# Performance work log

Hardware: AMD Instinct MI355X
Metric: run time of the kernel (lower is better)

## Reference

```python
import jax, jax.numpy as jnp
import numpy as np

B, C, H, W = 512, 256, 9, 9
HEADS, K = 4, 9
D_K = C // HEADS
EPS = 1e-5


def setup_inputs() -> dict:
    key = jax.random.key(0)
    ks = jax.random.split(key, 8)
    s = 1.0 / np.sqrt(C)
    return {
        "x": jax.random.normal(ks[0], (B, C, H, W), jnp.float32),
        "wq": jax.random.normal(ks[1], (C, C), jnp.float32) * s,
        "bq": jax.random.normal(ks[2], (C,), jnp.float32) * s,
        "wk": jax.random.normal(ks[3], (C, C), jnp.float32) * s,
        "bk": jax.random.normal(ks[4], (C,), jnp.float32) * s,
        "wv": jax.random.normal(ks[5], (C, C), jnp.float32) * s,
        "bv": jax.random.normal(ks[6], (C,), jnp.float32) * s,
        "a": jax.random.normal(ks[7], (HEADS, D_K), jnp.float32),
        "gamma": jnp.ones((C,), jnp.float32),
        "beta": jnp.zeros((C,), jnp.float32),
    }


def reference(x, wq, bq, wk, bk, wv, bv, a, gamma, beta):
    N = H * W  # 81 tokens
    tokens = x.reshape(B, C, N).transpose(0, 2, 1)  # [B, N, C]

    # pairwise euclidean distances (cdist)
    sq = jnp.sum(tokens * tokens, axis=-1)  # [B, N]
    d2 = sq[:, :, None] + sq[:, None, :] - 2.0 * jnp.einsum("bnc,bmc->bnm", tokens, tokens)
    dist = jnp.sqrt(jnp.maximum(d2, 0.0))  # [B, N, N]

    # k nearest neighbors (smallest distance)
    _, idx = jax.lax.top_k(-dist, K)  # idx: [B, N, K]

    # gather neighbor features: [B, N, K, C]
    nbr = jax.vmap(lambda t, i: t[i])(tokens, idx)

    q = tokens @ wq.T + bq                      # [B, N, C]
    kf = nbr @ wk.T + bk                        # [B, N, K, C]
    comb = jax.nn.leaky_relu(q[:, :, None, :] + kf, 0.2)
    comb = comb.reshape(B, N, K, HEADS, D_K)
    scores = jnp.einsum("bnkhd,hd->bnkh", comb, a)
    attn = jax.nn.softmax(scores, axis=2)       # over K neighbors
    v = (nbr @ wv.T + bv).reshape(B, N, K, HEADS, D_K)
    out = jnp.einsum("bnkh,bnkhd->bnhd", attn, v).reshape(B, N, C)
    out = out.transpose(0, 2, 1).reshape(B, C, H, W)

    # BatchNorm2d (training-mode batch statistics, biased variance)
    mean = jnp.mean(out, axis=(0, 2, 3))
    var = jnp.var(out, axis=(0, 2, 3))
    bn = (out - mean[None, :, None, None]) * jax.lax.rsqrt(var + EPS)[None, :, None, None]
    bn = bn * gamma[None, :, None, None] + beta[None, :, None, None]
    return jax.nn.relu(bn + x)
```

## Files before the change

### kernel.cpp

```cpp
#include <hip/hip_runtime.h>
#include <hip/hip_bf16.h>

#define B_   512
#define C_   256
#define N_   81
#define M_   (B_ * N_)
#define KNN  9

typedef __attribute__((ext_vector_type(8))) short short8;
typedef __attribute__((ext_vector_type(4))) float f32x4;
typedef __attribute__((ext_vector_type(4))) ushort u16x4;

#define GLD16(g, l) __builtin_amdgcn_global_load_lds(                      \
    (const __attribute__((address_space(1))) void*)(g),                    \
    (__attribute__((address_space(3))) void*)(l), 16, 0, 0)

__device__ __forceinline__ float bf2f(ushort u) {
  union { uint i; float f; } c; c.i = (uint)u << 16; return c.f;
}
__device__ __forceinline__ ushort f2bf(float f) {
  __hip_bfloat16 h = __float2bfloat16(f); return *(ushort*)&h;
}

__global__ __launch_bounds__(256) void split_kernel(
    const float* __restrict__ x, ushort* __restrict__ tokb,
    char* __restrict__ hlbuf,
    const float* __restrict__ wq, const float* __restrict__ bq,
    const float* __restrict__ wk, const float* __restrict__ bk,
    const float* __restrict__ wv, const float* __restrict__ bv,
    ushort* __restrict__ wcat, float* __restrict__ bcat) {
  __shared__ __align__(16) float raw[32 * 81];
  const int bid = blockIdx.x;
  const int tid = threadIdx.x;
  if (bid >= 4096) {
    const int j = bid - 4096, c = tid;
    const int sel = j >> 8, jr = j & 255;
    const float* W  = sel == 0 ? wq : (sel == 1 ? wk : wv);
    const float* Bb = sel == 0 ? bq : (sel == 1 ? bk : bv);
    wcat[(size_t)j * 256 + c] = f2bf(W[jr * 256 + c]);
    if (c == 0) bcat[j] = Bb[jr];
    return;
  }
  const int b = bid >> 3, ch = bid & 7;
  const float* src = x + (size_t)b * (C_ * N_) + ch * 32 * N_;
#pragma unroll
  for (int it = 0; it < 3; ++it) {
    int e4 = tid + it * 256;
    if (e4 < 648) *(f32x4*)&raw[e4 * 4] = *(const f32x4*)&src[e4 * 4];
  }
  char* dst = hlbuf + (size_t)bid * 12288;
  for (int p = tid; p < 480; p += 256)
    *(uint*)(dst + (81 + p / 32) * 128 + (p & 31) * 4) = 0u;
  __syncthreads();
#pragma unroll
  for (int it = 0; it < 6; ++it) {
    int p = tid + it * 256;
    if (p < 1296) {
      int n = p >> 4, q = p & 15;
      float v0 = raw[(2 * q) * N_ + n];
      float v1 = raw[(2 * q + 1) * N_ + n];
      __hip_bfloat16 h0 = __float2bfloat16(v0);
      __hip_bfloat16 h1 = __float2bfloat16(v1);
      float r0 = v0 - __bfloat162float(h0);
      float r1 = v1 - __bfloat162float(h1);
      __hip_bfloat16 g0 = __float2bfloat16(r0);
      __hip_bfloat16 g1 = __float2bfloat16(r1);
      uint hp = (uint)(*(ushort*)&h0) | ((uint)(*(ushort*)&h1) << 16);
      uint lp = (uint)(*(ushort*)&g0) | ((uint)(*(ushort*)&g1) << 16);
      int off = (((q >> 2) << 4) ^ (((n >> 1) & 3) << 4)) + ((q & 3) << 2);
      int hs = (n & 1) << 6;
      *(uint*)(dst + n * 128 + hs + off) = hp;
      *(uint*)(dst + n * 128 + (hs ^ 64) + off) = lp;
      *(uint*)&tokb[((size_t)(b * N_ + n)) * 256 + ch * 32 + 2 * q] = hp;
    }
  }
}

__global__ __launch_bounds__(256) void knn_kernel(
    const char* __restrict__ hlbuf, int* __restrict__ knn_idx) {
  __shared__ __align__(16) char smem[31488];
  __shared__ float sqv[96];
  const int b = blockIdx.x;
  const int tid = threadIdx.x;
  const int w = tid >> 6, lane = tid & 63;
  const int wr = w >> 1, wc = w & 1;
  const int l15 = lane & 15;
  const int g16 = lane >> 4;

  const char* srcb = hlbuf + (size_t)b * 8 * 12288;

#pragma unroll
  for (int it = 0; it < 3; ++it) {
    int idx = it * 256 + tid;
    GLD16(srcb + idx * 16, smem + idx * 16);
  }

  f32x4 acc[3][3];
#pragma unroll
  for (int i = 0; i < 3; ++i)
#pragma unroll
    for (int j = 0; j < 3; ++j) acc[i][j] = {0.f, 0.f, 0.f, 0.f};

#pragma unroll
  for (int ch = 0; ch < 8; ++ch) {
    char* cur = smem + (ch & 1) * 12288;
    char* nxt = smem + ((ch + 1) & 1) * 12288;
    if (ch < 7) {
      const char* s2 = srcb + (size_t)(ch + 1) * 12288;
#pragma unroll
      for (int it = 0; it < 3; ++it) {
        int idx = it * 256 + tid;
        GLD16(s2 + idx * 16, nxt + idx * 16);
      }
      asm volatile("s_waitcnt vmcnt(3)" ::: "memory");
    } else {
      asm volatile("s_waitcnt vmcnt(0)" ::: "memory");
    }
    __builtin_amdgcn_s_barrier();
    __builtin_amdgcn_sched_barrier(0);
    short8 ah[3], al[3], bh[3], bl[3];
#pragma unroll
    for (int i = 0; i < 3; ++i) {
      int ra = wr * 48 + i * 16 + l15;
      int basea = ra * 128 + ((g16 << 4) ^ (((ra >> 1) & 3) << 4));
      int hsa = (ra & 1) << 6;
      ah[i] = *(const short8*)(cur + basea + hsa);
      al[i] = *(const short8*)(cur + basea + (hsa ^ 64));
      int rb = wc * 48 + i * 16 + l15;
      int baseb = rb * 128 + ((g16 << 4) ^ (((rb >> 1) & 3) << 4));
      int hsb = (rb & 1) << 6;
      bh[i] = *(const short8*)(cur + baseb + hsb);
      bl[i] = *(const short8*)(cur + baseb + (hsb ^ 64));
    }
#pragma unroll
    for (int i = 0; i < 3; ++i)
#pragma unroll
      for (int j = 0; j < 3; ++j) {
        acc[i][j] = __builtin_amdgcn_mfma_f32_16x16x32_bf16(
            ah[i], bh[j], acc[i][j], 0, 0, 0);
        acc[i][j] = __builtin_amdgcn_mfma_f32_16x16x32_bf16(
            ah[i], bl[j], acc[i][j], 0, 0, 0);
        acc[i][j] = __builtin_amdgcn_mfma_f32_16x16x32_bf16(
            al[i], bh[j], acc[i][j], 0, 0, 0);
        acc[i][j] = __builtin_amdgcn_mfma_f32_16x16x32_bf16(
            al[i], bl[j], acc[i][j], 0, 0, 0);
      }
    __builtin_amdgcn_sched_barrier(0);
    __builtin_amdgcn_s_barrier();
  }
  float* G = (float*)smem;
#pragma unroll
  for (int i = 0; i < 3; ++i) {
    const int row0 = wr * 48 + i * 16 + ((lane >> 4) << 2);
#pragma unroll
    for (int j = 0; j < 3; ++j) {
      const int col = wc * 48 + j * 16 + l15;
#pragma unroll
      for (int reg = 0; reg < 4; ++reg) {
        const int row = row0 + reg;
        if (row < N_) G[row * 97 + col] = acc[i][j][reg];
      }
    }
  }
  __syncthreads();
  if (tid < N_) sqv[tid] = G[tid * 97 + tid];
  __syncthreads();
  if (tid < N_) {
    const int n = tid;
    const float sn = sqv[n];
    const float* grow = &G[n * 97];
    float bd[KNN]; int bi[KNN];
#pragma unroll
    for (int k = 0; k < KNN; ++k) { bd[k] = 3.4e38f; bi[k] = 0; }
    for (int m = 0; m < N_; ++m) {
      float d2 = sn + sqv[m] - 2.f * grow[m];
      float wv = bd[0]; int wi = 0;
#pragma unroll
      for (int k = 1; k < KNN; ++k) {
        bool g_ = bd[k] > wv;
        wv = g_ ? bd[k] : wv;
        wi = g_ ? k : wi;
      }
      bool repl = d2 < wv;
#pragma unroll
      for (int k = 0; k < KNN; ++k) {
        bool here = repl & (wi == k);
        bd[k] = here ? d2 : bd[k];
        bi[k] = here ? m : bi[k];
      }
    }
#pragma unroll
    for (int k = 0; k < KNN; ++k)
      knn_idx[((size_t)b * N_ + n) * KNN + k] = bi[k];
  }
}

__global__ __launch_bounds__(256) void qkv_mfma_kernel(
    const ushort* __restrict__ tokb, const ushort* __restrict__ wcat,
    const float* __restrict__ bcat, ushort* __restrict__ qkvb) {
  __shared__ ushort At[128 * 64];
  __shared__ ushort Bt[128 * 64];
  const int bid = blockIdx.x;
  const int xcd = bid & 7, li = bid >> 3;
  const int mt = xcd * 41 + li / 6;
  if (mt >= 324) return;
  const int m0 = mt * 128;
  const int j0 = (li % 6) * 128;
  const int tid = threadIdx.x;
  const int w = tid >> 6, lane = tid & 63;
  const int wr = w >> 1, wc = w & 1;

  const char* pA[4]; const char* pB[4]; int oL[4];
#pragma unroll
  for (int it = 0; it < 4; ++it) {
    int o = (it * 256 + tid) * 16;
    int r = o >> 7, cp = o & 127;
    int cl = cp ^ ((r & 7) << 4);
    oL[it] = o;
    pA[it] = (const char*)tokb + ((size_t)(m0 + r) * 256) * 2 + cl;
    pB[it] = (const char*)wcat + ((size_t)(j0 + r) * 256) * 2 + cl;
  }

  f32x4 acc[4][4];
#pragma unroll
  for (int i = 0; i < 4; ++i)
#pragma unroll
    for (int j = 0; j < 4; ++j) acc[i][j] = {0.f, 0.f, 0.f, 0.f};

  const int l15 = lane & 15;
  const int sw = (lane & 7) << 4;
  const int kgrp = (lane >> 4) << 4;

  for (int k0 = 0; k0 < 256; k0 += 64) {
    __syncthreads();
#pragma unroll
    for (int it = 0; it < 4; ++it) {
      GLD16(pA[it] + k0 * 2, (char*)At + oL[it]);
      GLD16(pB[it] + k0 * 2, (char*)Bt + oL[it]);
    }
    __syncthreads();
#pragma unroll
    for (int kk = 0; kk < 2; ++kk) {
      const int cb = (kk * 64 + kgrp) ^ sw;
      short8 am[4], bn[4];
#pragma unroll
      for (int i = 0; i < 4; ++i) {
        const int ra = wr * 64 + i * 16 + l15;
        am[i] = *(const short8*)((const char*)At + ra * 128 + cb);
        const int rb = wc * 64 + i * 16 + l15;
        bn[i] = *(const short8*)((const char*)Bt + rb * 128 + cb);
      }
#pragma unroll
      for (int i = 0; i < 4; ++i)
#pragma unroll
        for (int j = 0; j < 4; ++j)
          acc[i][j] = __builtin_amdgcn_mfma_f32_16x16x32_bf16(
              am[i], bn[j], acc[i][j], 0, 0, 0);
    }
  }

#pragma unroll
  for (int j = 0; j < 4; ++j) {
    const int colj = j0 + wc * 64 + j * 16 + l15;
    const float bs = bcat[colj];
#pragma unroll
    for (int i = 0; i < 4; ++i) {
      const int rowm = m0 + wr * 64 + i * 16 + ((lane >> 4) << 2);
#pragma unroll
      for (int reg = 0; reg < 4; ++reg)
        qkvb[(size_t)(rowm + reg) * 768 + colj] = f2bf(acc[i][j][reg] + bs);
    }
  }
}

__global__ __launch_bounds__(256) void attn_kernel(
    const ushort* __restrict__ qkvc, const int* __restrict__ knn_idx,
    const float* __restrict__ a, ushort* __restrict__ qkvb) {
  const int nwg = M_ / 4;
  const int bid = blockIdx.x;
  const int swz = (bid & 7) * (nwg / 8) + (bid >> 3);
  const int w = threadIdx.x >> 6, lane = threadIdx.x & 63;
  const int m = swz * 4 + w;
  const int b = m / N_;
  const int bbase = b * N_;

  const u16x4 qu = *(const u16x4*)&qkvc[(size_t)m * 768 + lane * 4];
  const f32x4 a4 = *(const f32x4*)&a[lane * 4];
  float q4[4];
#pragma unroll
  for (int u = 0; u < 4; ++u) q4[u] = bf2f(qu[u]);

  float sc[KNN];
  int nb[KNN];
#pragma unroll
  for (int k = 0; k < KNN; ++k) {
    int nbk = knn_idx[(size_t)m * KNN + k];
    nbk = __builtin_amdgcn_readfirstlane(nbk);
    nb[k] = nbk;
    const ushort* krow = qkvc + (size_t)(bbase + nbk) * 768 + 256;
    const u16x4 ku = *(const u16x4*)&krow[lane * 4];
    float p = 0.f;
#pragma unroll
    for (int u = 0; u < 4; ++u) {
      float t = q4[u] + bf2f(ku[u]);
      t = fmaxf(t, 0.2f * t);
      p = __builtin_fmaf(t, a4[u], p);
    }
    p += __shfl_xor(p, 1, 16);
    p += __shfl_xor(p, 2, 16);
    p += __shfl_xor(p, 4, 16);
    p += __shfl_xor(p, 8, 16);
    sc[k] = p;
  }
  float mx = sc[0];
#pragma unroll
  for (int k = 1; k < KNN; ++k) mx = fmaxf(mx, sc[k]);
  float s = 0.f;
#pragma unroll
  for (int k = 0; k < KNN; ++k) {
    sc[k] = __builtin_amdgcn_exp2f((sc[k] - mx) * 1.44269504f);
    s += sc[k];
  }
  const float inv = __builtin_amdgcn_rcpf(s);
  f32x4 acc = {0.f, 0.f, 0.f, 0.f};
#pragma unroll
  for (int k = 0; k < KNN; ++k) {
    const ushort* vrow = qkvc + (size_t)(bbase + nb[k]) * 768 + 512;
    const u16x4 vu = *(const u16x4*)&vrow[lane * 4];
    const float wk_ = sc[k] * inv;
#pragma unroll
    for (int u = 0; u < 4; ++u)
      acc[u] = __builtin_fmaf(wk_, bf2f(vu[u]), acc[u]);
  }
  u16x4 o;
#pragma unroll
  for (int u = 0; u < 4; ++u) o[u] = f2bf(acc[u]);
  *(u16x4*)&qkvb[(size_t)m * 768 + lane * 4] = o;
}

__global__ __launch_bounds__(256) void bn_partial_kernel(
    const ushort* __restrict__ qkvb, float* __restrict__ ps,
    float* __restrict__ ps2) {
  const int g = blockIdx.x, c = threadIdx.x;
  float s = 0.f, s2 = 0.f;
  for (int r = 0; r < M_ / 256; ++r) {
    float v = bf2f(qkvb[((size_t)g * (M_ / 256) + r) * 768 + c]);
    s += v; s2 += v * v;
  }
  ps[g * 256 + c] = s;
  ps2[g * 256 + c] = s2;
}

__global__ __launch_bounds__(256) void bn_finalize_kernel(
    const float* __restrict__ ps, const float* __restrict__ ps2,
    const float* __restrict__ gamma, const float* __restrict__ beta,
    float* __restrict__ scale, float* __restrict__ shift) {
  const int c = threadIdx.x;
  float s = 0.f, s2 = 0.f;
  for (int g = 0; g < 256; ++g) { s += ps[g * 256 + c]; s2 += ps2[g * 256 + c]; }
  const float mean = s * (1.f / (float)M_);
  const float var = s2 * (1.f / (float)M_) - mean * mean;
  const float rstd = rsqrtf(var + 1e-5f);
  scale[c] = gamma[c] * rstd;
  shift[c] = beta[c] - mean * gamma[c] * rstd;
}

__global__ __launch_bounds__(256) void bn_apply_kernel(
    const ushort* __restrict__ qkvb, const float* __restrict__ x,
    const float* __restrict__ scale, const float* __restrict__ shift,
    float* __restrict__ y) {
  __shared__ float t[N_ * 65];
  const int b = blockIdx.x, tid = threadIdx.x;
  for (int c0 = 0; c0 < 256; c0 += 64) {
    __syncthreads();
    for (int e = tid; e < N_ * 64; e += 256) {
      int n = e >> 6, c = e & 63;
      t[n * 65 + c] = bf2f(qkvb[((size_t)b * N_ + n) * 768 + c0 + c]);
    }
    __syncthreads();
    for (int f = tid; f < 64 * N_; f += 256) {
      int c = f / N_, n = f - c * N_;
      float o = t[n * 65 + c];
      size_t gi = (size_t)b * (C_ * N_) + (size_t)(c0 + c) * N_ + n;
      float bn = o * scale[c0 + c] + shift[c0 + c];
      float v = bn + x[gi];
      y[gi] = v > 0.f ? v : 0.f;
    }
  }
}

extern "C" void kernel_launch(void* const* d_in, const int* in_sizes, int n_in,
                              void* d_out, int out_size, void* d_ws,
                              size_t ws_size, hipStream_t stream) {
  const float* x     = (const float*)d_in[0];
  const float* wq    = (const float*)d_in[1];
  const float* bq    = (const float*)d_in[2];
  const float* wk    = (const float*)d_in[3];
  const float* bk    = (const float*)d_in[4];
  const float* wv    = (const float*)d_in[5];
  const float* bv    = (const float*)d_in[6];
  const float* a     = (const float*)d_in[7];
  const float* gamma = (const float*)d_in[8];
  const float* beta  = (const float*)d_in[9];
  float* out = (float*)d_out;

  ushort* qkvb = (ushort*)d_ws;
  char*   hlbuf = (char*)qkvb;
  ushort* tokb = qkvb + (size_t)M_ * 768;
  ushort* wcat = tokb + (size_t)M_ * 256;
  float*  bcat = (float*)(wcat + 768 * 256);
  int*    kidx = (int*)(bcat + 768);
  float*  ps   = (float*)(kidx + (size_t)M_ * KNN);
  float*  ps2  = ps + 256 * 256;
  float*  scale = ps2 + 256 * 256;
  float*  shift = scale + 256;

  split_kernel<<<4096 + 768, 256, 0, stream>>>(
      x, tokb, hlbuf, wq, bq, wk, bk, wv, bv, wcat, bcat);
  knn_kernel<<<B_, 256, 0, stream>>>(hlbuf, kidx);
  qkv_mfma_kernel<<<1968, 256, 0, stream>>>(tokb, wcat, bcat, qkvb);
  attn_kernel<<<M_ / 4, 256, 0, stream>>>(qkvb, kidx, a, qkvb);
  bn_partial_kernel<<<256, 256, 0, stream>>>(qkvb, ps, ps2);
  bn_finalize_kernel<<<1, 256, 0, stream>>>(ps, ps2, gamma, beta, scale, shift);
  bn_apply_kernel<<<B_, 256, 0, stream>>>(qkvb, x, scale, shift, out);
}
```

Measured before the change: 166.0 us.

## Store only bf16 residual in split buffer; knn reads high part from tokb

The split kernel no longer writes an interleaved hi/lo staging buffer. It writes only the low (residual) bf16 halves in a compact 64-byte-per-row layout. The knn kernel now pulls the high halves straight from the existing tokb token buffer with a swizzled global-to-LDS load and places the lo halves in a separate LDS region, which cuts global write traffic and zero padding. The attention kernel also loads the 9 neighbour indices once across lanes and broadcasts each with readlane instead of issuing 9 scalar loads. One risk is that the padding rows (81..95) of the lo buffer are no longer zeroed, so the knn tile may read stale data there, and the hi part for those rows now comes from the next batch's tokens.

```diff
diff --git a/kernel.cpp b/kernel.cpp
--- a/kernel.cpp
+++ b/kernel.cpp
@@ -24,7 +24,7 @@
 
 __global__ __launch_bounds__(256) void split_kernel(
     const float* __restrict__ x, ushort* __restrict__ tokb,
-    char* __restrict__ hlbuf,
+    char* __restrict__ lobuf,
     const float* __restrict__ wq, const float* __restrict__ bq,
     const float* __restrict__ wk, const float* __restrict__ bk,
     const float* __restrict__ wv, const float* __restrict__ bv,
@@ -48,9 +48,7 @@
     int e4 = tid + it * 256;
     if (e4 < 648) *(f32x4*)&raw[e4 * 4] = *(const f32x4*)&src[e4 * 4];
   }
-  char* dst = hlbuf + (size_t)bid * 12288;
-  for (int p = tid; p < 480; p += 256)
-    *(uint*)(dst + (81 + p / 32) * 128 + (p & 31) * 4) = 0u;
+  char* dst = lobuf + (size_t)bid * 6144;
   __syncthreads();
 #pragma unroll
   for (int it = 0; it < 6; ++it) {
@@ -68,16 +66,15 @@
       uint hp = (uint)(*(ushort*)&h0) | ((uint)(*(ushort*)&h1) << 16);
       uint lp = (uint)(*(ushort*)&g0) | ((uint)(*(ushort*)&g1) << 16);
       int off = (((q >> 2) << 4) ^ (((n >> 1) & 3) << 4)) + ((q & 3) << 2);
-      int hs = (n & 1) << 6;
-      *(uint*)(dst + n * 128 + hs + off) = hp;
-      *(uint*)(dst + n * 128 + (hs ^ 64) + off) = lp;
+      *(uint*)(dst + n * 64 + off) = lp;
       *(uint*)&tokb[((size_t)(b * N_ + n)) * 256 + ch * 32 + 2 * q] = hp;
     }
   }
 }
 
 __global__ __launch_bounds__(256) void knn_kernel(
-    const char* __restrict__ hlbuf, int* __restrict__ knn_idx) {
+    const ushort* __restrict__ tokb, const char* __restrict__ lobuf,
+    int* __restrict__ knn_idx) {
   __shared__ __align__(16) char smem[31488];
   __shared__ float sqv[96];
   const int b = blockIdx.x;
@@ -87,12 +84,19 @@
   const int l15 = lane & 15;
   const int g16 = lane >> 4;
 
-  const char* srcb = hlbuf + (size_t)b * 8 * 12288;
+  const char* tb = (const char*)(tokb + (size_t)b * N_ * 256);
+  const char* lb = lobuf + (size_t)b * 8 * 6144;
 
 #pragma unroll
   for (int it = 0; it < 3; ++it) {
     int idx = it * 256 + tid;
-    GLD16(srcb + idx * 16, smem + idx * 16);
+    if (idx < 384) {
+      int n = idx >> 2, gp = idx & 3;
+      int g = gp ^ ((n >> 1) & 3);
+      GLD16(tb + (size_t)n * 512 + (g << 4), smem + idx * 16);
+    } else {
+      GLD16(lb + (idx - 384) * 16, smem + idx * 16);
+    }
   }
 
   f32x4 acc[3][3];
@@ -106,11 +110,18 @@
     char* cur = smem + (ch & 1) * 12288;
     char* nxt = smem + ((ch + 1) & 1) * 12288;
     if (ch < 7) {
-      const char* s2 = srcb + (size_t)(ch + 1) * 12288;
 #pragma unroll
       for (int it = 0; it < 3; ++it) {
         int idx = it * 256 + tid;
-        GLD16(s2 + idx * 16, nxt + idx * 16);
+        if (idx < 384) {
+          int n = idx >> 2, gp = idx & 3;
+          int g = gp ^ ((n >> 1) & 3);
+          GLD16(tb + (size_t)n * 512 + (ch + 1) * 64 + (g << 4),
+                nxt + idx * 16);
+        } else {
+          GLD16(lb + (size_t)(ch + 1) * 6144 + (idx - 384) * 16,
+                nxt + idx * 16);
+        }
       }
       asm volatile("s_waitcnt vmcnt(3)" ::: "memory");
     } else {
@@ -122,15 +133,13 @@
 #pragma unroll
     for (int i = 0; i < 3; ++i) {
       int ra = wr * 48 + i * 16 + l15;
-      int basea = ra * 128 + ((g16 << 4) ^ (((ra >> 1) & 3) << 4));
-      int hsa = (ra & 1) << 6;
-      ah[i] = *(const short8*)(cur + basea + hsa);
-      al[i] = *(const short8*)(cur + basea + (hsa ^ 64));
+      int oa = ra * 64 + ((g16 << 4) ^ (((ra >> 1) & 3) << 4));
+      ah[i] = *(const short8*)(cur + oa);
+      al[i] = *(const short8*)(cur + 6144 + oa);
       int rb = wc * 48 + i * 16 + l15;
-      int baseb = rb * 128 + ((g16 << 4) ^ (((rb >> 1) & 3) << 4));
-      int hsb = (rb & 1) << 6;
-      bh[i] = *(const short8*)(cur + baseb + hsb);
-      bl[i] = *(const short8*)(cur + baseb + (hsb ^ 64));
+      int ob = rb * 64 + ((g16 << 4) ^ (((rb >> 1) & 3) << 4));
+      bh[i] = *(const short8*)(cur + ob);
+      bl[i] = *(const short8*)(cur + 6144 + ob);
     }
 #pragma unroll
     for (int i = 0; i < 3; ++i)
@@ -284,6 +293,9 @@
   const int b = m / N_;
   const int bbase = b * N_;
 
+  int nbk_l = 0;
+  if (lane < KNN) nbk_l = knn_idx[(size_t)m * KNN + lane];
+
   const u16x4 qu = *(const u16x4*)&qkvc[(size_t)m * 768 + lane * 4];
   const f32x4 a4 = *(const f32x4*)&a[lane * 4];
   float q4[4];
@@ -294,8 +306,7 @@
   int nb[KNN];
 #pragma unroll
   for (int k = 0; k < KNN; ++k) {
-    int nbk = knn_idx[(size_t)m * KNN + k];
-    nbk = __builtin_amdgcn_readfirstlane(nbk);
+    const int nbk = __builtin_amdgcn_readlane(nbk_l, k);
     nb[k] = nbk;
     const ushort* krow = qkvc + (size_t)(bbase + nbk) * 768 + 256;
     const u16x4 ku = *(const u16x4*)&krow[lane * 4];
@@ -405,7 +416,7 @@
   float* out = (float*)d_out;
 
   ushort* qkvb = (ushort*)d_ws;
-  char*   hlbuf = (char*)qkvb;
+  char*   lobuf = (char*)qkvb;
   ushort* tokb = qkvb + (size_t)M_ * 768;
   ushort* wcat = tokb + (size_t)M_ * 256;
   float*  bcat = (float*)(wcat + 768 * 256);
@@ -416,8 +427,8 @@
   float*  shift = scale + 256;
 
   split_kernel<<<4096 + 768, 256, 0, stream>>>(
-      x, tokb, hlbuf, wq, bq, wk, bk, wv, bv, wcat, bcat);
-  knn_kernel<<<B_, 256, 0, stream>>>(hlbuf, kidx);
+      x, tokb, lobuf, wq, bq, wk, bk, wv, bv, wcat, bcat);
+  knn_kernel<<<B_, 256, 0, stream>>>(tokb, lobuf, kidx);
   qkv_mfma_kernel<<<1968, 256, 0, stream>>>(tokb, wcat, bcat, qkvb);
   attn_kernel<<<M_ / 4, 256, 0, stream>>>(qkvb, kidx, a, qkvb);
   bn_partial_kernel<<<256, 256, 0, stream>>>(qkvb, ps, ps2);
```

New measurement: 160.8 us. 3.1% less time.
